# Kernel optimization log

Measured on AMD Instinct MI355X. Metric: run time of the kernel, lower is better.

## Reference

```python
import jax, jax.numpy as jnp
import numpy as np

TOP_K = 90
TEMP = 0.04
EPS_LN = 1e-5

def _l2norm(x):
    n = jnp.linalg.norm(x, axis=-1, keepdims=True)
    return x / jnp.maximum(n, 1e-12)

def _layernorm(x, g, b):
    mu = jnp.mean(x, axis=-1, keepdims=True)
    var = jnp.mean((x - mu) ** 2, axis=-1, keepdims=True)
    return (x - mu) * jax.lax.rsqrt(var + EPS_LN) * g + b

def setup_inputs() -> dict:
    key = jax.random.key(0)
    ks = jax.random.split(key, 8)
    B, N, D, ES = 2048, 100000, 1024, 101
    H1, H2 = 256, 128
    inp = {
        "en_1024": jax.random.normal(ks[0], (B, D), jnp.float32),
        "en_db": jax.random.normal(ks[1], (N, D), jnp.float32),
        "es_db": jax.random.normal(ks[2], (N, D), jnp.float32),
        "sp_idx": jax.random.randint(ks[3], (ES,), 0, D),
        "W1": jax.random.normal(ks[4], (D + ES, H1), jnp.float32) * 0.02,
        "b1": jnp.zeros((H1,), jnp.float32),
        "g1": jnp.ones((H1,), jnp.float32),
        "be1": jnp.zeros((H1,), jnp.float32),
        "W2": jax.random.normal(ks[5], (H1, H2), jnp.float32) * 0.02,
        "b2": jnp.zeros((H2,), jnp.float32),
        "g2": jnp.ones((H2,), jnp.float32),
        "be2": jnp.zeros((H2,), jnp.float32),
        "W3": jax.random.normal(ks[6], (H2, ES), jnp.float32) * 0.02,
        "b3": jnp.zeros((ES,), jnp.float32),
    }
    return inp

def reference(en_1024, en_db, es_db, sp_idx, W1, b1, g1, be1, W2, b2, g2, be2, W3, b3):
    # --- retrieval: cosine sim + topk softmax + weighted gather-sum ---
    q = _l2norm(en_1024)            # (B, 1024)
    db = _l2norm(en_db)             # (N, 1024)
    sims = q @ db.T                 # (B, N)
    top_sims, top_idx = jax.lax.top_k(sims, TOP_K)      # (B, K)
    w = jax.nn.softmax(top_sims / TEMP, axis=-1)        # (B, K)
    gathered = es_db[top_idx]       # (B, K, 1024)
    es_retrieved_1024 = jnp.einsum('bk,bkd->bd', w, gathered)  # (B, 1024)
    es_retrieved_101 = es_retrieved_1024[:, sp_idx]     # (B, 101)
    # --- fusion MLP (residual correction) ---
    feat = jnp.concatenate([en_1024, es_retrieved_101], axis=-1)  # (B, 1125)
    h = jax.nn.gelu(_layernorm(feat @ W1 + b1, g1, be1), approximate=False)
    h = jax.nn.gelu(_layernorm(h @ W2 + b2, g2, be2), approximate=False)
    delta = h @ W3 + b3
    es_pred_101 = es_retrieved_101 + delta
    return (es_pred_101, es_retrieved_101, delta)
```

## Files before the change

### kernel.cpp

```cpp
#include <hip/hip_runtime.h>
#include <hip/hip_bf16.h>
#include <hip/hip_fp16.h>

typedef _Float16 f16;
typedef _Float16 f16x8 __attribute__((ext_vector_type(8)));
typedef float f32x4 __attribute__((ext_vector_type(4)));

#define B_ROWS 2048
#define N_DB   100000
#define D_DIM  1024
#define ES     101
#define H1D    256
#define H2D    128
#define TOPK   90
#define TKEEP  112
#define RS_LO  80
#define RS_N   32
#define TEMPV  0.04f
#define NTOT   100352
#define NT_ALL 392
#define ESS    104
#define CAP    1024
#define CNTS   16
#define RCAP   24
#define GTHR   0.085f

#define GLOAD16(g, l) __builtin_amdgcn_global_load_lds( \
    (const __attribute__((address_space(1))) unsigned int*)(g), \
    (__attribute__((address_space(3))) unsigned int*)(l), 16, 0, 0)

__global__ __launch_bounds__(256) void qnorm_kernel(const float* __restrict__ en,
                                                    f16* __restrict__ qh) {
  __shared__ float red[4];
  int b = blockIdx.x, t = threadIdx.x;
  float4 v = ((const float4*)(en + (size_t)b * D_DIM))[t];
  float ss = v.x * v.x + v.y * v.y + v.z * v.z + v.w * v.w;
  for (int o = 32; o; o >>= 1) ss += __shfl_xor(ss, o);
  if ((t & 63) == 0) red[t >> 6] = ss;
  __syncthreads();
  float tot = red[0] + red[1] + red[2] + red[3];
  float sc = 1.0f / fmaxf(sqrtf(tot), 1e-12f);
  f16* o = qh + (size_t)b * D_DIM + t * 4;
  o[0] = (f16)(v.x * sc); o[1] = (f16)(v.y * sc);
  o[2] = (f16)(v.z * sc); o[3] = (f16)(v.w * sc);
}

__global__ __launch_bounds__(256) void prep_kernel(const float* __restrict__ db,
                                                   f16* __restrict__ dbh,
                                                   const float* __restrict__ es,
                                                   const int* __restrict__ sp,
                                                   float* __restrict__ es_sub) {
  __shared__ float red[4];
  __shared__ float row[1024];
  __shared__ int sps[ES];
  int r = blockIdx.x, t = threadIdx.x;
  if (r >= N_DB) {
    f16 z[4] = {(f16)0.f, (f16)0.f, (f16)0.f, (f16)0.f};
    *(float2*)(dbh + (size_t)r * D_DIM + t * 4) = *(float2*)z;
    return;
  }
  float4 v = ((const float4*)(db + (size_t)r * D_DIM))[t];
  float ss = v.x * v.x + v.y * v.y + v.z * v.z + v.w * v.w;
  for (int o = 32; o; o >>= 1) ss += __shfl_xor(ss, o);
  if ((t & 63) == 0) red[t >> 6] = ss;
  if (t < ES) sps[t] = sp[t];
  ((float4*)row)[t] = ((const float4*)(es + (size_t)r * D_DIM))[t];
  __syncthreads();
  float tot = red[0] + red[1] + red[2] + red[3];
  float sc = 1.0f / fmaxf(sqrtf(tot), 1e-12f);
  f16 tmp[4] = {(f16)(v.x * sc), (f16)(v.y * sc), (f16)(v.z * sc), (f16)(v.w * sc)};
  *(float2*)(dbh + (size_t)r * D_DIM + t * 4) = *(float2*)tmp;
  if (t < ES) es_sub[(size_t)r * ESS + t] = row[sps[t]];
}

__global__ __launch_bounds__(512) void gemm_kernel(const f16* __restrict__ qh,
                                                   const f16* __restrict__ dbh,
                                                   float* __restrict__ cand_v,
                                                   int* __restrict__ cand_i,
                                                   int* __restrict__ cand_cnt) {
  __shared__ f16 As[256 * 64];
  __shared__ f16 Bs[256 * 64];
  int t = threadIdx.x;
  int lane = t & 63, wid = t >> 6;
  int wr = wid >> 2, wc = wid & 3;
  int l15 = lane & 15, l4 = lane >> 4;
  int id = blockIdx.x;
  int swz = (id & 7) * (gridDim.x >> 3) + (id >> 3);
  int bm = swz & 7, bn = swz >> 3;
  int m0 = bm * 256;
  int col0 = bn * 256;

  const f16* srcA[4]; const f16* srcB[4];
  int dstoff[4];
  #pragma unroll
  for (int i = 0; i < 4; ++i) {
    int L = i * 512 + t;
    int row = L >> 3;
    int colh = ((L & 7) * 8) ^ ((row & 7) << 3);
    srcA[i] = qh  + (size_t)(m0 + row) * D_DIM + colh;
    srcB[i] = dbh + (size_t)(col0 + row) * D_DIM + colh;
    dstoff[i] = L * 16;
  }

  f32x4 acc[8][4] = {};

  for (int kt = 0; kt < D_DIM; kt += 64) {
    #pragma unroll
    for (int i = 0; i < 4; ++i) {
      GLOAD16(srcA[i] + kt, (char*)As + dstoff[i]);
      GLOAD16(srcB[i] + kt, (char*)Bs + dstoff[i]);
    }
    __syncthreads();
    #pragma unroll
    for (int s = 0; s < 2; ++s) {
      f16x8 a[8], b[4];
      #pragma unroll
      for (int f = 0; f < 8; ++f) {
        int rowA = wr * 128 + f * 16 + l15;
        int offA = rowA * 128 + ((s * 64 + l4 * 16) ^ ((rowA & 7) << 4));
        a[f] = *(const f16x8*)((const char*)As + offA);
      }
      #pragma unroll
      for (int f = 0; f < 4; ++f) {
        int rowB = wc * 64 + f * 16 + l15;
        int offB = rowB * 128 + ((s * 64 + l4 * 16) ^ ((rowB & 7) << 4));
        b[f] = *(const f16x8*)((const char*)Bs + offB);
      }
      #pragma unroll
      for (int fm = 0; fm < 8; ++fm)
        #pragma unroll
        for (int fn = 0; fn < 4; ++fn)
          acc[fm][fn] = __builtin_amdgcn_mfma_f32_16x16x32_f16(a[fm], b[fn], acc[fm][fn], 0, 0, 0);
    }
    __syncthreads();
  }

  unsigned* rcnt = (unsigned*)As;
  float*    rvv  = (float*)As + 512;
  int*      rvi  = (int*)Bs;
  if (t < 256) rcnt[t] = 0;
  __syncthreads();
  #pragma unroll
  for (int fm = 0; fm < 8; ++fm)
    #pragma unroll
    for (int fn = 0; fn < 4; ++fn) {
      int gcol = col0 + wc * 64 + fn * 16 + l15;
      if (gcol >= N_DB) continue;
      #pragma unroll
      for (int r = 0; r < 4; ++r) {
        int lrow = wr * 128 + fm * 16 + l4 * 4 + r;
        float v = acc[fm][fn][r];
        if (v > GTHR) {
          unsigned p = atomicAdd(&rcnt[lrow], 1u);
          if (p < RCAP) { rvv[lrow * RCAP + p] = v; rvi[lrow * RCAP + p] = gcol; }
        }
      }
    }
  __syncthreads();
  if (t < 256) {
    unsigned k = rcnt[t]; if (k > RCAP) k = RCAP;
    if (k) {
      int m = m0 + t;
      int base = atomicAdd(&cand_cnt[(size_t)m * CNTS], (int)k);
      for (unsigned j = 0; j < k; ++j) {
        int p = base + (int)j;
        if (p < CAP) {
          cand_v[(size_t)m * CAP + p] = rvv[t * RCAP + j];
          cand_i[(size_t)m * CAP + p] = rvi[t * RCAP + j];
        }
      }
    }
  }
}

__device__ inline void bsort(float* cv, int* ci, int t, int cnt, int p2) {
  for (int i = t; i < p2; i += 256)
    if (i >= cnt) { cv[i] = -3e38f; ci[i] = 0x7fffffff; }
  for (int k = 2; k <= p2; k <<= 1)
    for (int j = k >> 1; j > 0; j >>= 1) {
      __syncthreads();
      for (int i = t; i < p2; i += 256) {
        int ixj = i ^ j;
        if (ixj > i) {
          float v1 = cv[i], v2 = cv[ixj];
          int i1 = ci[i], i2 = ci[ixj];
          bool aBeforeB = (v1 > v2) || (v1 == v2 && i1 < i2);
          bool dirAsc = (i & k) != 0;
          bool doSwap = dirAsc ? aBeforeB : !aBeforeB;
          if (doSwap) { cv[i] = v2; cv[ixj] = v1; ci[i] = i2; ci[ixj] = i1; }
        }
      }
    }
  __syncthreads();
}

__global__ __launch_bounds__(256) void topk_final_kernel(const float* __restrict__ cand_v,
                                                         const int* __restrict__ cand_i,
                                                         const int* __restrict__ cand_cnt,
                                                         float* __restrict__ sval,
                                                         int* __restrict__ sidx) {
  __shared__ float cv[CAP];
  __shared__ int   ci[CAP];
  int b = blockIdx.x, t = threadIdx.x;
  int nc = cand_cnt[(size_t)b * CNTS]; if (nc > CAP) nc = CAP;
  for (int i = t; i < nc; i += 256) {
    cv[i] = cand_v[(size_t)b * CAP + i];
    ci[i] = cand_i[(size_t)b * CAP + i];
  }
  __syncthreads();
  int p2 = 128; while (p2 < nc) p2 <<= 1;
  bsort(cv, ci, t, nc, p2);
  if (t < TKEEP) { sval[(size_t)b * TKEEP + t] = cv[t]; sidx[(size_t)b * TKEEP + t] = ci[t]; }
}

__global__ __launch_bounds__(256) void rescore_kernel(const float* __restrict__ en,
                                                      const float* __restrict__ db,
                                                      float* __restrict__ sval,
                                                      int* __restrict__ sidx) {
  __shared__ float qs[1024];
  __shared__ double wred[4];
  __shared__ double exv[RS_N];
  __shared__ int    exi[RS_N];
  int b = blockIdx.x, t = threadIdx.x;
  int lane = t & 63, wid = t >> 6;
  double nq2 = 0.0;
  for (int i = t; i < 1024; i += 256) {
    float v = en[(size_t)b * D_DIM + i];
    qs[i] = v;
    nq2 = fma((double)v, (double)v, nq2);
  }
  for (int o = 32; o; o >>= 1) nq2 += __shfl_xor(nq2, o);
  if (lane == 0) wred[wid] = nq2;
  __syncthreads();
  double nq2t = wred[0] + wred[1] + wred[2] + wred[3];
  double nq = sqrt(nq2t); if (nq < 1e-12) nq = 1e-12;
  for (int c = wid * 8; c < wid * 8 + 8; ++c) {
    int idx = sidx[(size_t)b * TKEEP + RS_LO + c];
    if (idx < 0 || idx >= N_DB) idx = 0;
    const float* dr = db + (size_t)idx * D_DIM;
    double dot = 0.0, nd2 = 0.0;
    #pragma unroll
    for (int j = 0; j < 16; ++j) {
      double dd = (double)dr[lane + j * 64];
      dot = fma((double)qs[lane + j * 64], dd, dot);
      nd2 = fma(dd, dd, nd2);
    }
    for (int o = 32; o; o >>= 1) { dot += __shfl_xor(dot, o); nd2 += __shfl_xor(nd2, o); }
    if (lane == 0) {
      double nd = sqrt(nd2); if (nd < 1e-12) nd = 1e-12;
      exv[c] = dot / (nq * nd);
      exi[c] = idx;
    }
  }
  __syncthreads();
  if (wid == 0) {
    double v = (lane < RS_N) ? exv[lane] : -1e300;
    int    i = (lane < RS_N) ? exi[lane] : 0x7fffffff;
    int rank = 0;
    for (int j = 0; j < RS_N; ++j) {
      double vj = __shfl(v, j);
      int    ij = __shfl(i, j);
      if (lane < RS_N && ((vj > v) || (vj == v && ij < i))) ++rank;
    }
    if (lane < RS_N) { exv[rank] = v; exi[rank] = i; }
  }
  __syncthreads();
  if (t < RS_N) {
    sval[(size_t)b * TKEEP + RS_LO + t] = (float)exv[t];
    sidx[(size_t)b * TKEEP + RS_LO + t] = exi[t];
  }
}

__global__ __launch_bounds__(128) void softgather_kernel(const float* __restrict__ sval,
                                                         const int* __restrict__ sidx,
                                                         const float* __restrict__ es_sub,
                                                         float* __restrict__ esr,
                                                         float* __restrict__ out_esr) {
  __shared__ float w[TOPK];
  __shared__ int id[TOPK];
  __shared__ float ssum;
  int b = blockIdx.x, t = threadIdx.x;
  if (t < TOPK) {
    float vmax = sval[b * TKEEP];
    w[t] = expf((sval[b * TKEEP + t] - vmax) / TEMPV);
    id[t] = sidx[b * TKEEP + t];
  }
  __syncthreads();
  if (t == 0) {
    float s = 0.f;
    for (int k = 0; k < TOPK; ++k) s += w[k];
    ssum = s;
  }
  __syncthreads();
  float inv = 1.0f / ssum;
  if (t < ES) {
    float acc = 0.f;
    for (int k = 0; k < TOPK; ++k) acc += w[k] * es_sub[(size_t)id[k] * ESS + t];
    acc *= inv;
    esr[b * ES + t] = acc;
    out_esr[b * ES + t] = acc;
  }
}

__global__ __launch_bounds__(256) void mlp_kernel(const float* __restrict__ en,
                                                  const float* __restrict__ esr,
                                                  const float* __restrict__ W1, const float* __restrict__ b1,
                                                  const float* __restrict__ g1, const float* __restrict__ be1,
                                                  const float* __restrict__ W2, const float* __restrict__ b2,
                                                  const float* __restrict__ g2, const float* __restrict__ be2,
                                                  const float* __restrict__ W3, const float* __restrict__ b3,
                                                  float* __restrict__ out) {
  __shared__ float feat[8][1128];
  __shared__ float h1s[8][H1D];
  __shared__ float h2s[8][H2D];
  int t = threadIdx.x;
  int b0 = blockIdx.x * 8;
  int wid = t >> 6, lane = t & 63;
  for (int r = 0; r < 8; ++r) {
    const float* src = en + (size_t)(b0 + r) * D_DIM;
    for (int i = t; i < 1024; i += 256) feat[r][i] = src[i];
    if (t < ES) feat[r][1024 + t] = esr[(b0 + r) * ES + t];
  }
  __syncthreads();
  float acc[8];
  #pragma unroll
  for (int r = 0; r < 8; ++r) acc[r] = b1[t];
  for (int k = 0; k < 1125; ++k) {
    float wv = W1[k * H1D + t];
    #pragma unroll
    for (int r = 0; r < 8; ++r) acc[r] += feat[r][k] * wv;
  }
  #pragma unroll
  for (int r = 0; r < 8; ++r) h1s[r][t] = acc[r];
  __syncthreads();
  for (int rr = 0; rr < 2; ++rr) {
    int r = wid + rr * 4;
    float s = 0.f, s2 = 0.f;
    for (int j = lane; j < H1D; j += 64) { float x = h1s[r][j]; s += x; s2 += x * x; }
    for (int o = 32; o; o >>= 1) { s += __shfl_xor(s, o); s2 += __shfl_xor(s2, o); }
    float mu = s / H1D, var = s2 / H1D - mu * mu, rs = rsqrtf(var + 1e-5f);
    for (int j = lane; j < H1D; j += 64) {
      float x = (h1s[r][j] - mu) * rs * g1[j] + be1[j];
      h1s[r][j] = 0.5f * x * (1.0f + erff(x * 0.70710678118654752f));
    }
  }
  __syncthreads();
  if (t < H2D) {
    float acc2[8];
    #pragma unroll
    for (int r = 0; r < 8; ++r) acc2[r] = b2[t];
    for (int k = 0; k < H1D; ++k) {
      float wv = W2[k * H2D + t];
      #pragma unroll
      for (int r = 0; r < 8; ++r) acc2[r] += h1s[r][k] * wv;
    }
    #pragma unroll
    for (int r = 0; r < 8; ++r) h2s[r][t] = acc2[r];
  }
  __syncthreads();
  for (int rr = 0; rr < 2; ++rr) {
    int r = wid + rr * 4;
    float s = 0.f, s2 = 0.f;
    for (int j = lane; j < H2D; j += 64) { float x = h2s[r][j]; s += x; s2 += x * x; }
    for (int o = 32; o; o >>= 1) { s += __shfl_xor(s, o); s2 += __shfl_xor(s2, o); }
    float mu = s / H2D, var = s2 / H2D - mu * mu, rs = rsqrtf(var + 1e-5f);
    for (int j = lane; j < H2D; j += 64) {
      float x = (h2s[r][j] - mu) * rs * g2[j] + be2[j];
      h2s[r][j] = 0.5f * x * (1.0f + erff(x * 0.70710678118654752f));
    }
  }
  __syncthreads();
  if (t < ES) {
    for (int r = 0; r < 8; ++r) {
      float a = b3[t];
      for (int k = 0; k < H2D; ++k) a += h2s[r][k] * W3[k * ES + t];
      float ev = esr[(b0 + r) * ES + t];
      out[(size_t)(b0 + r) * ES + t] = ev + a;
      out[2 * (size_t)B_ROWS * ES + (size_t)(b0 + r) * ES + t] = a;
    }
  }
}

extern "C" void kernel_launch(void* const* d_in, const int* in_sizes, int n_in,
                              void* d_out, int out_size, void* d_ws, size_t ws_size,
                              hipStream_t stream) {
  const float* en   = (const float*)d_in[0];
  const float* endb = (const float*)d_in[1];
  const float* esdb = (const float*)d_in[2];
  const int*   sp   = (const int*)d_in[3];
  const float* W1   = (const float*)d_in[4];
  const float* b1   = (const float*)d_in[5];
  const float* g1   = (const float*)d_in[6];
  const float* be1  = (const float*)d_in[7];
  const float* W2   = (const float*)d_in[8];
  const float* b2   = (const float*)d_in[9];
  const float* g2   = (const float*)d_in[10];
  const float* be2  = (const float*)d_in[11];
  const float* W3   = (const float*)d_in[12];
  const float* b3   = (const float*)d_in[13];
  float* out = (float*)d_out;

  char* ws = (char*)d_ws;
  size_t off = 0;
  auto alloc = [&](size_t bytes) -> void* {
    void* p = ws + off;
    off += (bytes + 255) & ~(size_t)255;
    return p;
  };
  f16*   qh     = (f16*)  alloc((size_t)B_ROWS * D_DIM * sizeof(f16));
  f16*   dbh    = (f16*)  alloc((size_t)NTOT * D_DIM * sizeof(f16));
  float* sval   = (float*)alloc((size_t)B_ROWS * TKEEP * sizeof(float));
  int*   sidx   = (int*)  alloc((size_t)B_ROWS * TKEEP * sizeof(int));
  float* cand_v = (float*)alloc((size_t)B_ROWS * CAP * sizeof(float));
  int*   cand_i = (int*)  alloc((size_t)B_ROWS * CAP * sizeof(int));
  int*   cand_cnt = (int*)alloc((size_t)B_ROWS * CNTS * sizeof(int));
  float* es_sub = (float*)alloc((size_t)N_DB * ESS * sizeof(float));
  float* esr    = (float*)alloc((size_t)B_ROWS * ES * sizeof(float));
  (void)ws_size; (void)in_sizes; (void)n_in; (void)out_size;

  hipMemsetAsync(cand_cnt, 0, (size_t)B_ROWS * CNTS * sizeof(int), stream);
  hipLaunchKernelGGL(qnorm_kernel, dim3(B_ROWS), dim3(256), 0, stream, en, qh);
  hipLaunchKernelGGL(prep_kernel, dim3(NTOT), dim3(256), 0, stream, endb, dbh, esdb, sp, es_sub);
  hipLaunchKernelGGL(gemm_kernel, dim3(NT_ALL * 8), dim3(512), 0, stream,
                     qh, dbh, cand_v, cand_i, cand_cnt);
  hipLaunchKernelGGL(topk_final_kernel, dim3(B_ROWS), dim3(256), 0, stream,
                     cand_v, cand_i, cand_cnt, sval, sidx);
  hipLaunchKernelGGL(rescore_kernel, dim3(B_ROWS), dim3(256), 0, stream, en, endb, sval, sidx);
  hipLaunchKernelGGL(softgather_kernel, dim3(B_ROWS), dim3(128), 0, stream,
                     sval, sidx, es_sub, esr, out + (size_t)B_ROWS * ES);
  hipLaunchKernelGGL(mlp_kernel, dim3(B_ROWS / 8), dim3(256), 0, stream,
                     en, esr, W1, b1, g1, be1, W2, b2, g2, be2, W3, b3, out);
}
```

Baseline: 1.058 ms.

## Switch similarity GEMM to int8 MFMA with per-row scales and full exact rescore

Quantizes query and database rows to int8 with per-row absmax scales and runs the candidate-filter GEMM with int8 MFMA instructions, applying the row scales in the epilogue before thresholding. This halves operand bytes and doubles MFMA throughput per instruction. To cover the coarser int8 similarities, the rescore kernel now recomputes exact fp64 cosine for all 128 kept candidates, not only the boundary 32, and re-sorts them. That adds gather and compute work in rescore, and the threshold filter may drop true top-k candidates under the noisier int8 scores.

```diff
diff --git a/kernel.cpp b/kernel.cpp
--- a/kernel.cpp
+++ b/kernel.cpp
@@ -2,8 +2,7 @@
 #include <hip/hip_bf16.h>
 #include <hip/hip_fp16.h>
 
-typedef _Float16 f16;
-typedef _Float16 f16x8 __attribute__((ext_vector_type(8)));
+typedef int i32x4 __attribute__((ext_vector_type(4)));
 typedef float f32x4 __attribute__((ext_vector_type(4)));
 
 #define B_ROWS 2048
@@ -13,9 +12,7 @@
 #define H1D    256
 #define H2D    128
 #define TOPK   90
-#define TKEEP  112
-#define RS_LO  80
-#define RS_N   32
+#define TKEEP  128
 #define TEMPV  0.04f
 #define NTOT   100352
 #define NT_ALL 392
@@ -29,57 +26,75 @@
     (const __attribute__((address_space(1))) unsigned int*)(g), \
     (__attribute__((address_space(3))) unsigned int*)(l), 16, 0, 0)
 
+__device__ inline int q8clamp(float x) {
+  int q = (int)rintf(x);
+  return q < -127 ? -127 : (q > 127 ? 127 : q);
+}
+
 __global__ __launch_bounds__(256) void qnorm_kernel(const float* __restrict__ en,
-                                                    f16* __restrict__ qh) {
-  __shared__ float red[4];
+                                                    char* __restrict__ qa,
+                                                    float* __restrict__ fa) {
+  __shared__ float red[4], redm[4];
   int b = blockIdx.x, t = threadIdx.x;
   float4 v = ((const float4*)(en + (size_t)b * D_DIM))[t];
   float ss = v.x * v.x + v.y * v.y + v.z * v.z + v.w * v.w;
-  for (int o = 32; o; o >>= 1) ss += __shfl_xor(ss, o);
-  if ((t & 63) == 0) red[t >> 6] = ss;
+  float mx = fmaxf(fmaxf(fabsf(v.x), fabsf(v.y)), fmaxf(fabsf(v.z), fabsf(v.w)));
+  for (int o = 32; o; o >>= 1) { ss += __shfl_xor(ss, o); mx = fmaxf(mx, __shfl_xor(mx, o)); }
+  if ((t & 63) == 0) { red[t >> 6] = ss; redm[t >> 6] = mx; }
   __syncthreads();
   float tot = red[0] + red[1] + red[2] + red[3];
-  float sc = 1.0f / fmaxf(sqrtf(tot), 1e-12f);
-  f16* o = qh + (size_t)b * D_DIM + t * 4;
-  o[0] = (f16)(v.x * sc); o[1] = (f16)(v.y * sc);
-  o[2] = (f16)(v.z * sc); o[3] = (f16)(v.w * sc);
+  float mtot = fmaxf(fmaxf(redm[0], redm[1]), fmaxf(redm[2], redm[3]));
+  float s = fmaxf(mtot, 1e-30f) / 127.0f;
+  float rs = 1.0f / s;
+  if (t == 0) fa[b] = s / fmaxf(sqrtf(tot), 1e-12f);
+  int packed = (q8clamp(v.x * rs) & 0xff) | ((q8clamp(v.y * rs) & 0xff) << 8) |
+               ((q8clamp(v.z * rs) & 0xff) << 16) | ((q8clamp(v.w * rs) & 0xff) << 24);
+  ((int*)(qa + (size_t)b * D_DIM))[t] = packed;
 }
 
 __global__ __launch_bounds__(256) void prep_kernel(const float* __restrict__ db,
-                                                   f16* __restrict__ dbh,
+                                                   char* __restrict__ qb,
+                                                   float* __restrict__ fb,
                                                    const float* __restrict__ es,
                                                    const int* __restrict__ sp,
                                                    float* __restrict__ es_sub) {
-  __shared__ float red[4];
+  __shared__ float red[4], redm[4];
   __shared__ float row[1024];
   __shared__ int sps[ES];
   int r = blockIdx.x, t = threadIdx.x;
   if (r >= N_DB) {
-    f16 z[4] = {(f16)0.f, (f16)0.f, (f16)0.f, (f16)0.f};
-    *(float2*)(dbh + (size_t)r * D_DIM + t * 4) = *(float2*)z;
+    ((int*)(qb + (size_t)r * D_DIM))[t] = 0;
+    if (t == 0) fb[r] = 0.f;
     return;
   }
   float4 v = ((const float4*)(db + (size_t)r * D_DIM))[t];
   float ss = v.x * v.x + v.y * v.y + v.z * v.z + v.w * v.w;
-  for (int o = 32; o; o >>= 1) ss += __shfl_xor(ss, o);
-  if ((t & 63) == 0) red[t >> 6] = ss;
+  float mx = fmaxf(fmaxf(fabsf(v.x), fabsf(v.y)), fmaxf(fabsf(v.z), fabsf(v.w)));
+  for (int o = 32; o; o >>= 1) { ss += __shfl_xor(ss, o); mx = fmaxf(mx, __shfl_xor(mx, o)); }
+  if ((t & 63) == 0) { red[t >> 6] = ss; redm[t >> 6] = mx; }
   if (t < ES) sps[t] = sp[t];
   ((float4*)row)[t] = ((const float4*)(es + (size_t)r * D_DIM))[t];
   __syncthreads();
   float tot = red[0] + red[1] + red[2] + red[3];
-  float sc = 1.0f / fmaxf(sqrtf(tot), 1e-12f);
-  f16 tmp[4] = {(f16)(v.x * sc), (f16)(v.y * sc), (f16)(v.z * sc), (f16)(v.w * sc)};
-  *(float2*)(dbh + (size_t)r * D_DIM + t * 4) = *(float2*)tmp;
+  float mtot = fmaxf(fmaxf(redm[0], redm[1]), fmaxf(redm[2], redm[3]));
+  float s = fmaxf(mtot, 1e-30f) / 127.0f;
+  float rs = 1.0f / s;
+  if (t == 0) fb[r] = s / fmaxf(sqrtf(tot), 1e-12f);
+  int packed = (q8clamp(v.x * rs) & 0xff) | ((q8clamp(v.y * rs) & 0xff) << 8) |
+               ((q8clamp(v.z * rs) & 0xff) << 16) | ((q8clamp(v.w * rs) & 0xff) << 24);
+  ((int*)(qb + (size_t)r * D_DIM))[t] = packed;
   if (t < ES) es_sub[(size_t)r * ESS + t] = row[sps[t]];
 }
 
-__global__ __launch_bounds__(512) void gemm_kernel(const f16* __restrict__ qh,
-                                                   const f16* __restrict__ dbh,
+__global__ __launch_bounds__(512) void gemm_kernel(const char* __restrict__ qa,
+                                                   const char* __restrict__ qb,
+                                                   const float* __restrict__ fav,
+                                                   const float* __restrict__ fbv,
                                                    float* __restrict__ cand_v,
                                                    int* __restrict__ cand_i,
                                                    int* __restrict__ cand_cnt) {
-  __shared__ f16 As[256 * 64];
-  __shared__ f16 Bs[256 * 64];
+  __shared__ char As[256 * 128];
+  __shared__ char Bs[256 * 128];
   int t = threadIdx.x;
   int lane = t & 63, wid = t >> 6;
   int wr = wid >> 2, wc = wid & 3;
@@ -90,66 +105,74 @@
   int m0 = bm * 256;
   int col0 = bn * 256;
 
-  const f16* srcA[4]; const f16* srcB[4];
+  const char* srcA[4]; const char* srcB[4];
   int dstoff[4];
   #pragma unroll
   for (int i = 0; i < 4; ++i) {
     int L = i * 512 + t;
     int row = L >> 3;
-    int colh = ((L & 7) * 8) ^ ((row & 7) << 3);
-    srcA[i] = qh  + (size_t)(m0 + row) * D_DIM + colh;
-    srcB[i] = dbh + (size_t)(col0 + row) * D_DIM + colh;
+    int colb = ((L & 7) * 16) ^ ((row & 7) << 4);
+    srcA[i] = qa + (size_t)(m0 + row) * D_DIM + colb;
+    srcB[i] = qb + (size_t)(col0 + row) * D_DIM + colb;
     dstoff[i] = L * 16;
   }
 
-  f32x4 acc[8][4] = {};
-
-  for (int kt = 0; kt < D_DIM; kt += 64) {
+  i32x4 acc[8][4] = {};
+
+  for (int kt = 0; kt < D_DIM; kt += 128) {
     #pragma unroll
     for (int i = 0; i < 4; ++i) {
-      GLOAD16(srcA[i] + kt, (char*)As + dstoff[i]);
-      GLOAD16(srcB[i] + kt, (char*)Bs + dstoff[i]);
+      GLOAD16(srcA[i] + kt, As + dstoff[i]);
+      GLOAD16(srcB[i] + kt, Bs + dstoff[i]);
     }
     __syncthreads();
     #pragma unroll
     for (int s = 0; s < 2; ++s) {
-      f16x8 a[8], b[4];
+      i32x4 a[8], b[4];
       #pragma unroll
       for (int f = 0; f < 8; ++f) {
         int rowA = wr * 128 + f * 16 + l15;
         int offA = rowA * 128 + ((s * 64 + l4 * 16) ^ ((rowA & 7) << 4));
-        a[f] = *(const f16x8*)((const char*)As + offA);
+        a[f] = *(const i32x4*)(As + offA);
       }
       #pragma unroll
       for (int f = 0; f < 4; ++f) {
         int rowB = wc * 64 + f * 16 + l15;
         int offB = rowB * 128 + ((s * 64 + l4 * 16) ^ ((rowB & 7) << 4));
-        b[f] = *(const f16x8*)((const char*)Bs + offB);
+        b[f] = *(const i32x4*)(Bs + offB);
       }
       #pragma unroll
       for (int fm = 0; fm < 8; ++fm)
         #pragma unroll
         for (int fn = 0; fn < 4; ++fn)
-          acc[fm][fn] = __builtin_amdgcn_mfma_f32_16x16x32_f16(a[fm], b[fn], acc[fm][fn], 0, 0, 0);
+          acc[fm][fn] = __builtin_amdgcn_mfma_i32_16x16x64_i8(a[fm], b[fn], acc[fm][fn], 0, 0, 0);
     }
     __syncthreads();
   }
 
-  unsigned* rcnt = (unsigned*)As;
-  float*    rvv  = (float*)As + 512;
+  float* fa_l = (float*)As;
+  float* fb_l = (float*)As + 256;
+  unsigned* rcnt = (unsigned*)As + 512;
+  float*    rvv  = (float*)As + 1024;
   int*      rvi  = (int*)Bs;
-  if (t < 256) rcnt[t] = 0;
+  if (t < 256) {
+    fa_l[t] = fav[m0 + t];
+    fb_l[t] = (col0 + t < N_DB) ? fbv[col0 + t] : 0.f;
+    rcnt[t] = 0;
+  }
   __syncthreads();
   #pragma unroll
   for (int fm = 0; fm < 8; ++fm)
     #pragma unroll
     for (int fn = 0; fn < 4; ++fn) {
-      int gcol = col0 + wc * 64 + fn * 16 + l15;
+      int ncl = wc * 64 + fn * 16 + l15;
+      int gcol = col0 + ncl;
       if (gcol >= N_DB) continue;
+      float fbn = fb_l[ncl];
       #pragma unroll
       for (int r = 0; r < 4; ++r) {
         int lrow = wr * 128 + fm * 16 + l4 * 4 + r;
-        float v = acc[fm][fn][r];
+        float v = (float)acc[fm][fn][r] * fa_l[lrow] * fbn;
         if (v > GTHR) {
           unsigned p = atomicAdd(&rcnt[lrow], 1u);
           if (p < RCAP) { rvv[lrow * RCAP + p] = v; rvi[lrow * RCAP + p] = gcol; }
@@ -219,8 +242,8 @@
                                                       int* __restrict__ sidx) {
   __shared__ float qs[1024];
   __shared__ double wred[4];
-  __shared__ double exv[RS_N];
-  __shared__ int    exi[RS_N];
+  __shared__ float cv[TKEEP];
+  __shared__ int   ci[TKEEP];
   int b = blockIdx.x, t = threadIdx.x;
   int lane = t & 63, wid = t >> 6;
   double nq2 = 0.0;
@@ -234,8 +257,8 @@
   __syncthreads();
   double nq2t = wred[0] + wred[1] + wred[2] + wred[3];
   double nq = sqrt(nq2t); if (nq < 1e-12) nq = 1e-12;
-  for (int c = wid * 8; c < wid * 8 + 8; ++c) {
-    int idx = sidx[(size_t)b * TKEEP + RS_LO + c];
+  for (int c = wid * 32; c < wid * 32 + 32; ++c) {
+    int idx = sidx[(size_t)b * TKEEP + c];
     if (idx < 0 || idx >= N_DB) idx = 0;
     const float* dr = db + (size_t)idx * D_DIM;
     double dot = 0.0, nd2 = 0.0;
@@ -248,26 +271,15 @@
     for (int o = 32; o; o >>= 1) { dot += __shfl_xor(dot, o); nd2 += __shfl_xor(nd2, o); }
     if (lane == 0) {
       double nd = sqrt(nd2); if (nd < 1e-12) nd = 1e-12;
-      exv[c] = dot / (nq * nd);
-      exi[c] = idx;
-    }
-  }
-  __syncthreads();
-  if (wid == 0) {
-    double v = (lane < RS_N) ? exv[lane] : -1e300;
-    int    i = (lane < RS_N) ? exi[lane] : 0x7fffffff;
-    int rank = 0;
-    for (int j = 0; j < RS_N; ++j) {
-      double vj = __shfl(v, j);
-      int    ij = __shfl(i, j);
-      if (lane < RS_N && ((vj > v) || (vj == v && ij < i))) ++rank;
-    }
-    if (lane < RS_N) { exv[rank] = v; exi[rank] = i; }
-  }
-  __syncthreads();
-  if (t < RS_N) {
-    sval[(size_t)b * TKEEP + RS_LO + t] = (float)exv[t];
-    sidx[(size_t)b * TKEEP + RS_LO + t] = exi[t];
+      cv[c] = (float)(dot / (nq * nd));
+      ci[c] = idx;
+    }
+  }
+  __syncthreads();
+  bsort(cv, ci, t, TKEEP, TKEEP);
+  if (t < TKEEP) {
+    sval[(size_t)b * TKEEP + t] = cv[t];
+    sidx[(size_t)b * TKEEP + t] = ci[t];
   }
 }
 
@@ -281,9 +293,9 @@
   __shared__ float ssum;
   int b = blockIdx.x, t = threadIdx.x;
   if (t < TOPK) {
-    float vmax = sval[b * TKEEP];
-    w[t] = expf((sval[b * TKEEP + t] - vmax) / TEMPV);
-    id[t] = sidx[b * TKEEP + t];
+    float vmax = sval[(size_t)b * TKEEP];
+    w[t] = expf((sval[(size_t)b * TKEEP + t] - vmax) / TEMPV);
+    id[t] = sidx[(size_t)b * TKEEP + t];
   }
   __syncthreads();
   if (t == 0) {
@@ -407,8 +419,10 @@
     off += (bytes + 255) & ~(size_t)255;
     return p;
   };
-  f16*   qh     = (f16*)  alloc((size_t)B_ROWS * D_DIM * sizeof(f16));
-  f16*   dbh    = (f16*)  alloc((size_t)NTOT * D_DIM * sizeof(f16));
+  char*  qa     = (char*) alloc((size_t)B_ROWS * D_DIM);
+  char*  qb     = (char*) alloc((size_t)NTOT * D_DIM);
+  float* fa     = (float*)alloc((size_t)B_ROWS * sizeof(float));
+  float* fb     = (float*)alloc((size_t)NTOT * sizeof(float));
   float* sval   = (float*)alloc((size_t)B_ROWS * TKEEP * sizeof(float));
   int*   sidx   = (int*)  alloc((size_t)B_ROWS * TKEEP * sizeof(int));
   float* cand_v = (float*)alloc((size_t)B_ROWS * CAP * sizeof(float));
@@ -419,10 +433,10 @@
   (void)ws_size; (void)in_sizes; (void)n_in; (void)out_size;
 
   hipMemsetAsync(cand_cnt, 0, (size_t)B_ROWS * CNTS * sizeof(int), stream);
-  hipLaunchKernelGGL(qnorm_kernel, dim3(B_ROWS), dim3(256), 0, stream, en, qh);
-  hipLaunchKernelGGL(prep_kernel, dim3(NTOT), dim3(256), 0, stream, endb, dbh, esdb, sp, es_sub);
+  hipLaunchKernelGGL(qnorm_kernel, dim3(B_ROWS), dim3(256), 0, stream, en, qa, fa);
+  hipLaunchKernelGGL(prep_kernel, dim3(NTOT), dim3(256), 0, stream, endb, qb, fb, esdb, sp, es_sub);
   hipLaunchKernelGGL(gemm_kernel, dim3(NT_ALL * 8), dim3(512), 0, stream,
-                     qh, dbh, cand_v, cand_i, cand_cnt);
+                     qa, qb, fa, fb, cand_v, cand_i, cand_cnt);
   hipLaunchKernelGGL(topk_final_kernel, dim3(B_ROWS), dim3(256), 0, stream,
                      cand_v, cand_i, cand_cnt, sval, sidx);
   hipLaunchKernelGGL(rescore_kernel, dim3(B_ROWS), dim3(256), 0, stream, en, endb, sval, sidx);
```

Measured after the change: 966.4 us. -8.7%, faster.
